# Kernel tuning notes

Measured on AMD Instinct MI355X. Metric: run time of the kernel, lower is better.

The kernel has to match this reference:

```python
import jax, jax.numpy as jnp
import numpy as np

N, E, F_IN, H1, H2, C, G = 100000, 1600000, 128, 128, 64, 10, 64

def setup_inputs() -> dict:
    key = jax.random.key(0)
    ks = jax.random.split(key, 10)
    x = jax.random.normal(ks[0], (N, F_IN), dtype=jnp.float32)
    edge_index = jax.random.randint(ks[1], (2, E), 0, N, dtype=jnp.int32)
    batch = jnp.sort(jax.random.randint(ks[2], (N,), 0, G, dtype=jnp.int32))
    W1 = jax.random.normal(ks[3], (F_IN, H1), dtype=jnp.float32) * 0.05
    b1 = jnp.zeros((H1,), dtype=jnp.float32)
    W2 = jax.random.normal(ks[4], (H1, H2), dtype=jnp.float32) * 0.05
    b2 = jnp.zeros((H2,), dtype=jnp.float32)
    Wfc = jax.random.normal(ks[5], (H2, C), dtype=jnp.float32) * 0.05
    bfc = jnp.zeros((C,), dtype=jnp.float32)
    return {"x": x, "edge_index": edge_index, "batch": batch,
            "W1": W1, "b1": b1, "W2": W2, "b2": b2, "Wfc": Wfc, "bfc": bfc}

def gcn_conv(x, src, dst, W, b, n_nodes):
    # PyG GCNConv: add self-loops, symmetric normalization D^-1/2 A D^-1/2, linear, bias
    h = x @ W  # [N, H]
    deg = jnp.zeros((n_nodes,), h.dtype).at[dst].add(1.0) + 1.0  # +1 self-loop
    dinv = jax.lax.rsqrt(deg)
    norm = dinv[src] * dinv[dst]  # [E]
    msg = h[src] * norm[:, None]  # gather + scale
    agg = jnp.zeros_like(h).at[dst].add(msg)  # scatter-add at target
    agg = agg + h * (dinv * dinv)[:, None]    # self-loop messages
    return agg + b

def global_mean_pool(x, batch, num_graphs):
    sums = jnp.zeros((num_graphs, x.shape[1]), x.dtype).at[batch].add(x)
    cnt = jnp.zeros((num_graphs,), x.dtype).at[batch].add(1.0)
    return sums / jnp.maximum(cnt, 1.0)[:, None]

def reference(x, edge_index, batch, W1, b1, W2, b2, Wfc, bfc):
    src, dst = edge_index[0], edge_index[1]
    h = gcn_conv(x, src, dst, W1, b1, N)
    h = jax.nn.relu(h)
    # dropout is identity in eval mode
    h = gcn_conv(h, src, dst, W2, b2, N)
    g = global_mean_pool(h, batch, G)  # [G, 64]
    return g @ Wfc + bfc  # [G, C]
```

## Files before the change

kernel.cpp:

```cpp
#include <hip/hip_runtime.h>
#include <cstdint>

#define NN   100000
#define NE   1600000
#define FIN  128
#define HH1  128
#define HH2  64
#define NC   10
#define NG   64

#define NB   256
#define NPB  392
#define BCAP 8192
#define EPB  8192
#define NBLK_B ((NE + EPB - 1) / EPB)

typedef __attribute__((ext_vector_type(8))) short bf16x8;
typedef __attribute__((ext_vector_type(4))) float f32x4;
typedef __attribute__((ext_vector_type(2))) float f32x2;

#if defined(__has_builtin)
#  if __has_builtin(__builtin_amdgcn_cvt_pk_f32_fp8) && \
      __has_builtin(__builtin_amdgcn_cvt_f32_fp8) && \
      __has_builtin(__builtin_amdgcn_cvt_pk_fp8_f32)
#    define HW_FP8 1
#  endif
#endif
#ifndef HW_FP8
#  define HW_FP8 0
#endif

__device__ __forceinline__ unsigned pack2(float a, float b) {
    union { float f; unsigned u; } x, y; x.f = a; y.f = b;
    const unsigned lo = x.u + 0x7fffu + ((x.u >> 16) & 1u);
    const unsigned hi = y.u + 0x7fffu + ((y.u >> 16) & 1u);
    return (lo >> 16) | (hi & 0xffff0000u);
}

__device__ __forceinline__ float sw_dec8(unsigned b) {
    const unsigned s = b >> 7, e = (b >> 3) & 15u, m = b & 7u;
    float v;
    if (e == 0) v = (float)m * 0.001953125f;
    else { union { unsigned u; float f; } y; y.u = ((e + 120u) << 23) | (m << 20); v = y.f; }
    return s ? -v : v;
}
__device__ __forceinline__ unsigned sw_enc8(float f) {
    union { float f; unsigned u; } x; x.f = f;
    const unsigned s = (x.u >> 31) << 7;
    float a = fabsf(f);
    a = fminf(a, 448.0f);
    unsigned ia;
    if (a < 0.015625f) {
        ia = (unsigned)(int)rintf(a * 512.0f);
    } else {
        union { float f; unsigned u; } y; y.f = a;
        int e = (int)((y.u >> 23) & 255u) - 127;
        unsigned keep = (y.u >> 20) & 7u;
        const unsigned rest = y.u & 0xfffffu;
        keep += (rest > 0x80000u) || (rest == 0x80000u && (keep & 1u));
        if (keep == 8u) { keep = 0u; e += 1; }
        if (e >= 8) { e = 8; if (keep > 6u) keep = 6u; }
        ia = ((unsigned)(e + 7) << 3) | keep;
    }
    return s | ia;
}
__device__ __forceinline__ f32x4 fp8x4_f32(unsigned u) {
#if HW_FP8
    f32x2 lo = __builtin_amdgcn_cvt_pk_f32_fp8(u, false);
    f32x2 hi = __builtin_amdgcn_cvt_pk_f32_fp8(u, true);
    return (f32x4){lo[0], lo[1], hi[0], hi[1]};
#else
    return (f32x4){sw_dec8(u & 0xffu), sw_dec8((u >> 8) & 0xffu),
                   sw_dec8((u >> 16) & 0xffu), sw_dec8(u >> 24)};
#endif
}
__device__ __forceinline__ float fp8_f32(unsigned b) {
#if HW_FP8
    return __builtin_amdgcn_cvt_f32_fp8(b, 0);
#else
    return sw_dec8(b & 0xffu);
#endif
}
__device__ __forceinline__ unsigned f32_fp8(float a) {
#if HW_FP8
    return __builtin_amdgcn_cvt_pk_fp8_f32(a, a, 0u, false) & 0xffu;
#else
    return sw_enc8(a);
#endif
}
__device__ __forceinline__ unsigned pack4_fp8(float a, float b, float c, float d) {
#if HW_FP8
    unsigned u = __builtin_amdgcn_cvt_pk_fp8_f32(a, b, 0u, false);
    u = __builtin_amdgcn_cvt_pk_fp8_f32(c, d, u, true);
    return u;
#else
    return sw_enc8(a) | (sw_enc8(b) << 8) | (sw_enc8(c) << 16) | (sw_enc8(d) << 24);
#endif
}

__global__ __launch_bounds__(256) void k_init(int* __restrict__ gcursor,
                                              float* __restrict__ sums) {
    const int i = blockIdx.x * blockDim.x + threadIdx.x;
    if (i < NB) gcursor[i] = i * BCAP;
    if (i < NG * HH2 + NG) sums[i] = 0.f;
}

__global__ __launch_bounds__(256) void k_bscatter(const int* __restrict__ src,
                                                  const int* __restrict__ dst,
                                                  int* __restrict__ gcursor,
                                                  unsigned* __restrict__ pairs, int E) {
    __shared__ int cnt[NB];
    __shared__ int cur[NB];
    const int t = threadIdx.x;
    cnt[t] = 0;
    __syncthreads();
    const int base = blockIdx.x * EPB;
#pragma unroll
    for (int i = 0; i < EPB / 1024; ++i) {
        const int e = base + i * 1024 + t * 4;
        if (e < E) {
            const int4 d = *(const int4*)&dst[e];
            atomicAdd(&cnt[(unsigned)d.x / NPB], 1);
            atomicAdd(&cnt[(unsigned)d.y / NPB], 1);
            atomicAdd(&cnt[(unsigned)d.z / NPB], 1);
            atomicAdd(&cnt[(unsigned)d.w / NPB], 1);
        }
    }
    __syncthreads();
    {
        const int c = cnt[t];
        if (c) cur[t] = atomicAdd(&gcursor[t], c);
    }
    __syncthreads();
#pragma unroll
    for (int i = 0; i < EPB / 1024; ++i) {
        const int e = base + i * 1024 + t * 4;
        if (e < E) {
            const int4 d = *(const int4*)&dst[e];
            const int4 s = *(const int4*)&src[e];
            int p; unsigned bk, lo;
            bk = (unsigned)d.x / NPB; lo = d.x - bk * NPB;
            p = atomicAdd(&cur[bk], 1); pairs[p] = ((unsigned)s.x << 9) | lo;
            bk = (unsigned)d.y / NPB; lo = d.y - bk * NPB;
            p = atomicAdd(&cur[bk], 1); pairs[p] = ((unsigned)s.y << 9) | lo;
            bk = (unsigned)d.z / NPB; lo = d.z - bk * NPB;
            p = atomicAdd(&cur[bk], 1); pairs[p] = ((unsigned)s.z << 9) | lo;
            bk = (unsigned)d.w / NPB; lo = d.w - bk * NPB;
            p = atomicAdd(&cur[bk], 1); pairs[p] = ((unsigned)s.w << 9) | lo;
        }
    }
}

__global__ __launch_bounds__(512) void k_csr(const unsigned* __restrict__ pairs,
                                             const int* __restrict__ gcursor,
                                             int* __restrict__ row_start,
                                             int* __restrict__ rend,
                                             float* __restrict__ dinv,
                                             int* __restrict__ esrc) {
    const int b = blockIdx.x;
    const int node0 = b * NPB;
    if (node0 >= NN) return;
    const int nn = min(NPB, NN - node0);
    __shared__ int cnt[NPB];
    __shared__ int scn[512];
    __shared__ int cur[NPB];
    const int t = threadIdx.x;
    if (t < NPB) cnt[t] = 0;
    __syncthreads();
    const int ebeg = b * BCAP, eend = gcursor[b];
    for (int j = ebeg + t; j < eend; j += 512)
        atomicAdd(&cnt[pairs[j] & 511u], 1);
    __syncthreads();
    const int v = (t < nn) ? cnt[t] : 0;
    const int pv = (v + 3) & ~3;
    scn[t] = pv;
    __syncthreads();
    for (int off = 1; off < 512; off <<= 1) {
        const int x = (t >= off) ? scn[t - off] : 0;
        __syncthreads();
        scn[t] += x;
        __syncthreads();
    }
    if (t < nn) {
        const int rs = ebeg + scn[t] - pv;
        row_start[node0 + t] = rs;
        rend[node0 + t]      = rs + v;
        cur[t] = rs;
        dinv[node0 + t] = rsqrtf((float)v + 1.f);
    }
    __syncthreads();
    for (int j = ebeg + t; j < eend; j += 512) {
        const unsigned p = pairs[j];
        const int pos = atomicAdd(&cur[p & 511u], 1);
        esrc[pos] = (int)(p >> 9);
    }
}

template <int BN, bool ABF16>
__global__ __launch_bounds__(256) void k_mfma(const void* __restrict__ Ain,
                                              const float* __restrict__ Bin,
                                              unsigned char* __restrict__ Cout,
                                              const float* __restrict__ rowscale,
                                              int M) {
    __shared__ unsigned short Bs[BN][128];
    const int t = threadIdx.x;
    const int row0 = blockIdx.x * 128;

    {
        constexpr int KSEG = (BN == 128) ? 64 : 32;
        const int n  = t & (BN - 1);
        const int kb = (t / BN) * KSEG;
#pragma unroll
        for (int i = 0; i < KSEG; i += 2) {
            const int k = kb + i;
            const unsigned u = pack2(Bin[(size_t)k * BN + n], Bin[(size_t)(k + 1) * BN + n]);
            *(unsigned*)&Bs[n][(((k >> 3) ^ (n & 7)) << 3) + (k & 7)] = u;
        }
    }

    const int lane = t & 63, wave = t >> 6;
    const int lr = lane & 15, lg = lane >> 4;
    constexpr int MR = 2;
    constexpr int NR = BN / 16;
    const int wrow = wave * 32;

    bf16x8 afrag[4][MR];
#pragma unroll
    for (int m = 0; m < MR; ++m) {
        int row = row0 + wrow + m * 16 + lr;
        row = (row < M) ? row : (M - 1);
        if (ABF16) {
            const uint4* ap = (const uint4*)((const unsigned short*)Ain + (size_t)row * 128);
#pragma unroll
            for (int ks = 0; ks < 4; ++ks) {
                const uint4 v = ap[ks * 4 + lg];
                afrag[ks][m] = *(const bf16x8*)&v;
            }
        } else {
            const float* ap = (const float*)Ain + (size_t)row * 128;
#pragma unroll
            for (int ks = 0; ks < 4; ++ks) {
                const float4 f0 = *(const float4*)(ap + ks * 32 + lg * 8);
                const float4 f1 = *(const float4*)(ap + ks * 32 + lg * 8 + 4);
                const uint4 v = make_uint4(pack2(f0.x, f0.y), pack2(f0.z, f0.w),
                                           pack2(f1.x, f1.y), pack2(f1.z, f1.w));
                afrag[ks][m] = *(const bf16x8*)&v;
            }
        }
    }
    __syncthreads();

    f32x4 acc[MR][NR];
#pragma unroll
    for (int m = 0; m < MR; ++m)
#pragma unroll
        for (int n = 0; n < NR; ++n) acc[m][n] = (f32x4){0.f, 0.f, 0.f, 0.f};

#pragma unroll
    for (int ks = 0; ks < 4; ++ks) {
        const int cc = ((ks * 4 + lg) ^ (lr & 7)) * 8;
        bf16x8 b[NR];
#pragma unroll
        for (int n = 0; n < NR; ++n) b[n] = *(const bf16x8*)&Bs[n * 16 + lr][cc];
#pragma unroll
        for (int m = 0; m < MR; ++m)
#pragma unroll
            for (int n = 0; n < NR; ++n)
                acc[m][n] = __builtin_amdgcn_mfma_f32_16x16x32_bf16(afrag[ks][m], b[n], acc[m][n], 0, 0, 0);
    }

#pragma unroll
    for (int m = 0; m < MR; ++m) {
        const int rb = wrow + m * 16 + lg * 4;
        float s[4]; int gr[4];
#pragma unroll
        for (int j = 0; j < 4; ++j) {
            gr[j] = row0 + rb + j;
            s[j] = (gr[j] < M) ? rowscale[gr[j]] : 0.f;
        }
#pragma unroll
        for (int n = 0; n < NR; ++n) {
            const int col = n * 16 + lr;
#pragma unroll
            for (int j = 0; j < 4; ++j)
                if (gr[j] < M)
                    Cout[(size_t)gr[j] * BN + col] = (unsigned char)f32_fp8(acc[m][n][j] * s[j]);
        }
    }
}

__global__ __launch_bounds__(256) void k_agg1(const int* __restrict__ row_start,
                                              const int* __restrict__ row_end,
                                              const int* __restrict__ esrc,
                                              const float* __restrict__ dinv,
                                              const uint2* __restrict__ hb,
                                              const float* __restrict__ b,
                                              uint4* __restrict__ outp, int n) {
    const int wid  = (blockIdx.x * blockDim.x + threadIdx.x) >> 6;
    const int lane = threadIdx.x & 63;
    if (wid >= n) return;
    const int q  = lane >> 4;
    const int ql = lane & 15;
    const int beg = row_start[wid], end = row_end[wid];

    f32x4 accA = (f32x4){0.f, 0.f, 0.f, 0.f};
    f32x4 accB = accA;
    if (q == 0) {
        const uint2 u = hb[(size_t)wid * 16 + ql];
        accA = fp8x4_f32(u.x);
        accB = fp8x4_f32(u.y);
    }

    int j = beg;
    for (; j + 16 <= end; j += 16) {
        const int4 ix = *(const int4*)&esrc[j + q * 4];
        const uint2 u0 = hb[(size_t)ix.x * 16 + ql];
        const uint2 u1 = hb[(size_t)ix.y * 16 + ql];
        const uint2 u2 = hb[(size_t)ix.z * 16 + ql];
        const uint2 u3 = hb[(size_t)ix.w * 16 + ql];
        accA += (fp8x4_f32(u0.x) + fp8x4_f32(u1.x)) + (fp8x4_f32(u2.x) + fp8x4_f32(u3.x));
        accB += (fp8x4_f32(u0.y) + fp8x4_f32(u1.y)) + (fp8x4_f32(u2.y) + fp8x4_f32(u3.y));
    }
    for (; j + 4 <= end; j += 4) {
        const uint2 u = hb[(size_t)esrc[j + q] * 16 + ql];
        accA += fp8x4_f32(u.x);
        accB += fp8x4_f32(u.y);
    }
    if (j + q < end) {
        const uint2 u = hb[(size_t)esrc[j + q] * 16 + ql];
        accA += fp8x4_f32(u.x);
        accB += fp8x4_f32(u.y);
    }

#pragma unroll
    for (int k = 0; k < 4; ++k) {
        accA[k] += __shfl_xor(accA[k], 16); accA[k] += __shfl_xor(accA[k], 32);
        accB[k] += __shfl_xor(accB[k], 16); accB[k] += __shfl_xor(accB[k], 32);
    }

    if (q == 0) {
        const float dd = dinv[wid];
        const float4 bv0 = *(const float4*)&b[ql * 8];
        const float4 bv1 = *(const float4*)&b[ql * 8 + 4];
        float r[8];
        r[0] = fmaxf(fmaf(dd, accA[0], bv0.x), 0.f);
        r[1] = fmaxf(fmaf(dd, accA[1], bv0.y), 0.f);
        r[2] = fmaxf(fmaf(dd, accA[2], bv0.z), 0.f);
        r[3] = fmaxf(fmaf(dd, accA[3], bv0.w), 0.f);
        r[4] = fmaxf(fmaf(dd, accB[0], bv1.x), 0.f);
        r[5] = fmaxf(fmaf(dd, accB[1], bv1.y), 0.f);
        r[6] = fmaxf(fmaf(dd, accB[2], bv1.z), 0.f);
        r[7] = fmaxf(fmaf(dd, accB[3], bv1.w), 0.f);
        outp[(size_t)wid * 16 + ql] = make_uint4(pack2(r[0], r[1]), pack2(r[2], r[3]),
                                                 pack2(r[4], r[5]), pack2(r[6], r[7]));
    }
}

__global__ __launch_bounds__(256) void k_agg2(const int* __restrict__ row_start,
                                              const int* __restrict__ row_end,
                                              const int* __restrict__ esrc,
                                              const float* __restrict__ dinv,
                                              const uint2* __restrict__ hb,
                                              const float* __restrict__ b,
                                              uint2* __restrict__ outp, int n) {
    const int wid  = (blockIdx.x * blockDim.x + threadIdx.x) >> 6;
    const int lane = threadIdx.x & 63;
    if (wid >= n) return;
    const int o  = lane >> 3;
    const int ol = lane & 7;
    const int beg = row_start[wid], end = row_end[wid];

    f32x4 accA = (f32x4){0.f, 0.f, 0.f, 0.f};
    f32x4 accB = accA;
    if (o == 0) {
        const uint2 u = hb[(size_t)wid * 8 + ol];
        accA = fp8x4_f32(u.x);
        accB = fp8x4_f32(u.y);
    }

    int j = beg;
    for (; j + 16 <= end; j += 16) {
        const int2 ix = *(const int2*)&esrc[j + o * 2];
        const uint2 u0 = hb[(size_t)ix.x * 8 + ol];
        const uint2 u1 = hb[(size_t)ix.y * 8 + ol];
        accA += fp8x4_f32(u0.x) + fp8x4_f32(u1.x);
        accB += fp8x4_f32(u0.y) + fp8x4_f32(u1.y);
    }
    for (; j + 8 <= end; j += 8) {
        const uint2 u = hb[(size_t)esrc[j + o] * 8 + ol];
        accA += fp8x4_f32(u.x);
        accB += fp8x4_f32(u.y);
    }
    if (j + o < end) {
        const uint2 u = hb[(size_t)esrc[j + o] * 8 + ol];
        accA += fp8x4_f32(u.x);
        accB += fp8x4_f32(u.y);
    }

#pragma unroll
    for (int k = 0; k < 4; ++k) {
        accA[k] += __shfl_xor(accA[k], 8);
        accA[k] += __shfl_xor(accA[k], 16);
        accA[k] += __shfl_xor(accA[k], 32);
        accB[k] += __shfl_xor(accB[k], 8);
        accB[k] += __shfl_xor(accB[k], 16);
        accB[k] += __shfl_xor(accB[k], 32);
    }

    if (o == 0) {
        const float dd = dinv[wid];
        const float4 bv0 = *(const float4*)&b[ol * 8];
        const float4 bv1 = *(const float4*)&b[ol * 8 + 4];
        const unsigned w0 = pack4_fp8(fmaf(dd, accA[0], bv0.x), fmaf(dd, accA[1], bv0.y),
                                      fmaf(dd, accA[2], bv0.z), fmaf(dd, accA[3], bv0.w));
        const unsigned w1 = pack4_fp8(fmaf(dd, accB[0], bv1.x), fmaf(dd, accB[1], bv1.y),
                                      fmaf(dd, accB[2], bv1.z), fmaf(dd, accB[3], bv1.w));
        outp[(size_t)wid * 8 + ol] = make_uint2(w0, w1);
    }
}

__global__ __launch_bounds__(256) void k_pool(const unsigned char* __restrict__ v2,
                                              const int* __restrict__ batch,
                                              float* __restrict__ sums,
                                              float* __restrict__ cnt, int n) {
    constexpr int NPW = 128;
    const int gt = blockIdx.x * blockDim.x + threadIdx.x;
    const int wave = gt >> 6;
    const int lane = threadIdx.x & 63;
    const int start = wave * NPW;
    if (start >= n) return;
    const int end = min(start + NPW, n);
    float acc = 0.f, cacc = 0.f;
    int cur = batch[start];
    for (int nd = start; nd < end; ++nd) {
        const int gid = batch[nd];
        if (gid != cur) {
            atomicAdd(&sums[cur * HH2 + lane], acc);
            if (lane == 0) atomicAdd(&cnt[cur], cacc);
            acc = 0.f; cacc = 0.f; cur = gid;
        }
        acc += fp8_f32(v2[(size_t)nd * 64 + lane]);
        cacc += 1.f;
    }
    atomicAdd(&sums[cur * HH2 + lane], acc);
    if (lane == 0) atomicAdd(&cnt[cur], cacc);
}

__global__ void k_fc(const float* __restrict__ sums, const float* __restrict__ cnt,
                     const float* __restrict__ Wfc, const float* __restrict__ bfc,
                     float* __restrict__ out) {
    const int tid = threadIdx.x;
    if (tid >= NG * NC) return;
    const int g = tid / NC;
    const int c = tid % NC;
    float a = 0.f;
    for (int k = 0; k < HH2; ++k)
        a = fmaf(sums[g * HH2 + k], Wfc[k * NC + c], a);
    const float cg = fmaxf(cnt[g], 1.0f);
    out[g * NC + c] = a / cg + bfc[c];
}

extern "C" void kernel_launch(void* const* d_in, const int* in_sizes, int n_in,
                              void* d_out, int out_size, void* d_ws, size_t ws_size,
                              hipStream_t stream) {
    const float* x   = (const float*)d_in[0];
    const int*   ei  = (const int*)d_in[1];
    const int*   bat = (const int*)d_in[2];
    const float* W1  = (const float*)d_in[3];
    const float* b1  = (const float*)d_in[4];
    const float* W2  = (const float*)d_in[5];
    const float* b2  = (const float*)d_in[6];
    const float* Wfc = (const float*)d_in[7];
    const float* bfc = (const float*)d_in[8];
    float* out = (float*)d_out;

    const int* src = ei;
    const int* dst = ei + NE;

    float* ws = (float*)d_ws;
    unsigned* relu1     = (unsigned*)ws;
    unsigned char* v2   = (unsigned char*)ws;
    unsigned char* h1b  = (unsigned char*)(ws + (size_t)NN * 64);
    unsigned char* h2b  = (unsigned char*)(ws + (size_t)NN * 64);
    float*    dinv      = ws + (size_t)NN * 96;
    int*      row_start = (int*)(ws + (size_t)NN * 97);
    int*      rend      = (int*)(ws + (size_t)NN * 98);
    int*      esrc      = (int*)(ws + (size_t)NN * 99);
    unsigned* pairs     = (unsigned*)(ws + (size_t)NN * 99 + (size_t)NB * BCAP);
    float*    sums      = ws + (size_t)NN * 99 + 2 * (size_t)NB * BCAP;
    float*    cntf      = sums + NG * HH2;
    int*      gcursor   = (int*)(cntf + NG);

    k_init<<<(NG * HH2 + NG + 255) / 256, 256, 0, stream>>>(gcursor, sums);
    k_bscatter<<<NBLK_B, 256, 0, stream>>>(src, dst, gcursor, pairs, NE);
    k_csr<<<NB, 512, 0, stream>>>(pairs, gcursor, row_start, rend, dinv, esrc);

    const int gblk = (NN + 127) / 128;

    k_mfma<128, false><<<gblk, 256, 0, stream>>>(x, W1, h1b, dinv, NN);
    k_agg1<<<(NN * 64 + 255) / 256, 256, 0, stream>>>(row_start, rend, esrc, dinv,
                                                      (const uint2*)h1b, b1,
                                                      (uint4*)relu1, NN);

    k_mfma<64, true><<<gblk, 256, 0, stream>>>(relu1, W2, h2b, dinv, NN);
    k_agg2<<<(NN * 64 + 255) / 256, 256, 0, stream>>>(row_start, rend, esrc, dinv,
                                                      (const uint2*)h2b, b2,
                                                      (uint2*)v2, NN);

    {
        const int waves = (NN + 127) / 128;
        const int blocks = (waves * 64 + 255) / 256;
        k_pool<<<blocks, 256, 0, stream>>>(v2, bat, sums, cntf, NN);
    }

    k_fc<<<1, 640, 0, stream>>>(sums, cntf, Wfc, bfc, out);
}
```

Before: 223.4 us.

## Stage bucket scatter in shared memory to coalesce global pair writes

The edge bucketing kernel now reads each edge once, keeps values and local bucket offsets in registers, and computes a block-wide prefix scan of the bucket counts. It then writes the edges into a shared-memory staging buffer sorted by bucket and flushes them to global memory in bucket order, so the global writes become more contiguous. Edges per block drop from 8192 to 4096 to fit the staging buffers. This removes the second read of src/dst and the scattered global stores, at the cost of more shared memory per block, a scan with many barriers, and twice as many global cursor atomics.

Measured after the change: 221.4 us, median of 2. No clear change (-0.9%).

```diff
diff --git a/kernel.cpp b/kernel.cpp
--- a/kernel.cpp
+++ b/kernel.cpp
@@ -12,8 +12,8 @@
 #define NB   256
 #define NPB  392
 #define BCAP 8192
-#define EPB  8192
-#define NBLK_B ((NE + EPB - 1) / EPB)
+#define EPS  4096
+#define NBLK_B ((NE + EPS - 1) / EPS)
 
 typedef __attribute__((ext_vector_type(8))) short bf16x8;
 typedef __attribute__((ext_vector_type(4))) float f32x4;
@@ -110,45 +110,67 @@
                                                   int* __restrict__ gcursor,
                                                   unsigned* __restrict__ pairs, int E) {
     __shared__ int cnt[NB];
-    __shared__ int cur[NB];
+    __shared__ int lst[NB];
+    __shared__ int bglob[NB];
+    __shared__ unsigned buf[EPS];
+    __shared__ int gd[EPS];
     const int t = threadIdx.x;
     cnt[t] = 0;
     __syncthreads();
-    const int base = blockIdx.x * EPB;
-#pragma unroll
-    for (int i = 0; i < EPB / 1024; ++i) {
-        const int e = base + i * 1024 + t * 4;
-        if (e < E) {
-            const int4 d = *(const int4*)&dst[e];
-            atomicAdd(&cnt[(unsigned)d.x / NPB], 1);
-            atomicAdd(&cnt[(unsigned)d.y / NPB], 1);
-            atomicAdd(&cnt[(unsigned)d.z / NPB], 1);
-            atomicAdd(&cnt[(unsigned)d.w / NPB], 1);
-        }
-    }
-    __syncthreads();
-    {
-        const int c = cnt[t];
-        if (c) cur[t] = atomicAdd(&gcursor[t], c);
-    }
-    __syncthreads();
-#pragma unroll
-    for (int i = 0; i < EPB / 1024; ++i) {
+    const int base = blockIdx.x * EPS;
+    unsigned val[16]; int bo[16];
+#pragma unroll
+    for (int i = 0; i < 4; ++i) {
         const int e = base + i * 1024 + t * 4;
         if (e < E) {
             const int4 d = *(const int4*)&dst[e];
             const int4 s = *(const int4*)&src[e];
-            int p; unsigned bk, lo;
-            bk = (unsigned)d.x / NPB; lo = d.x - bk * NPB;
-            p = atomicAdd(&cur[bk], 1); pairs[p] = ((unsigned)s.x << 9) | lo;
-            bk = (unsigned)d.y / NPB; lo = d.y - bk * NPB;
-            p = atomicAdd(&cur[bk], 1); pairs[p] = ((unsigned)s.y << 9) | lo;
-            bk = (unsigned)d.z / NPB; lo = d.z - bk * NPB;
-            p = atomicAdd(&cur[bk], 1); pairs[p] = ((unsigned)s.z << 9) | lo;
-            bk = (unsigned)d.w / NPB; lo = d.w - bk * NPB;
-            p = atomicAdd(&cur[bk], 1); pairs[p] = ((unsigned)s.w << 9) | lo;
-        }
-    }
+            unsigned bk;
+            bk = (unsigned)d.x / NPB;
+            val[i * 4 + 0] = ((unsigned)s.x << 9) | ((unsigned)d.x - bk * NPB);
+            bo[i * 4 + 0] = (int)((bk << 16) | (unsigned)atomicAdd(&cnt[bk], 1));
+            bk = (unsigned)d.y / NPB;
+            val[i * 4 + 1] = ((unsigned)s.y << 9) | ((unsigned)d.y - bk * NPB);
+            bo[i * 4 + 1] = (int)((bk << 16) | (unsigned)atomicAdd(&cnt[bk], 1));
+            bk = (unsigned)d.z / NPB;
+            val[i * 4 + 2] = ((unsigned)s.z << 9) | ((unsigned)d.z - bk * NPB);
+            bo[i * 4 + 2] = (int)((bk << 16) | (unsigned)atomicAdd(&cnt[bk], 1));
+            bk = (unsigned)d.w / NPB;
+            val[i * 4 + 3] = ((unsigned)s.w << 9) | ((unsigned)d.w - bk * NPB);
+            bo[i * 4 + 3] = (int)((bk << 16) | (unsigned)atomicAdd(&cnt[bk], 1));
+        } else {
+            bo[i * 4 + 0] = bo[i * 4 + 1] = bo[i * 4 + 2] = bo[i * 4 + 3] = -1;
+        }
+    }
+    __syncthreads();
+    const int v = cnt[t];
+    lst[t] = v;
+    __syncthreads();
+    for (int off = 1; off < 256; off <<= 1) {
+        const int x = (t >= off) ? lst[t - off] : 0;
+        __syncthreads();
+        lst[t] += x;
+        __syncthreads();
+    }
+    const int total = lst[NB - 1];
+    const int excl = lst[t] - v;
+    if (v > 0) bglob[t] = atomicAdd(&gcursor[t], v);
+    __syncthreads();
+    lst[t] = excl;
+    __syncthreads();
+#pragma unroll
+    for (int i = 0; i < 16; ++i) {
+        if (bo[i] >= 0) {
+            const int bk = bo[i] >> 16;
+            const int r  = bo[i] & 0xffff;
+            const int pos = lst[bk] + r;
+            buf[pos] = val[i];
+            gd[pos]  = bglob[bk] + r;
+        }
+    }
+    __syncthreads();
+    for (int p = t; p < total; p += 256)
+        pairs[gd[p]] = buf[p];
 }
 
 __global__ __launch_bounds__(512) void k_csr(const unsigned* __restrict__ pairs,
```
